# Kernel tuning notes

Hardware: AMD Instinct MI355X
Metric: run time of the kernel (lower is better)

## Reference

```python
import jax, jax.numpy as jnp
import numpy as np

B, TQ, TV, DQ, DV, UNITS = 4, 512, 1024, 256, 256, 64


def setup_inputs() -> dict:
    key = jax.random.key(0)
    k1, k2, k3, k4, k5 = jax.random.split(key, 5)
    return {
        "query": jax.random.normal(k1, (B, TQ, DQ), dtype=jnp.float32),
        "value": jax.random.normal(k2, (B, TV, DV), dtype=jnp.float32),
        "w1": jax.random.normal(k3, (DQ, UNITS), dtype=jnp.float32) / np.sqrt(DQ),
        "w2": jax.random.normal(k4, (DV, UNITS), dtype=jnp.float32) / np.sqrt(DV),
        "scale": jax.random.normal(k5, (UNITS,), dtype=jnp.float32),
    }


def reference(query, value, w1, w2, scale):
    # Dense projections (no bias)
    q = jnp.einsum('bqd,du->bqu', query, w1)   # [B,Tq,U]
    k = jnp.einsum('bvd,du->bvu', value, w2)   # [B,Tv,U]
    # Keras AdditiveAttention (use_scale=True):
    # scores[b,q,v] = sum_u scale[u] * tanh(q[b,q,u] + k[b,v,u])
    scores = jnp.einsum('bqvu,u->bqv',
                        jnp.tanh(q[:, :, None, :] + k[:, None, :, :]), scale)
    attn = jax.nn.softmax(scores, axis=-1)      # [B,Tq,Tv]
    context = jnp.einsum('bqv,bvd->bqd', attn, value)  # [B,Tq,Dv]
    return context, attn
```

## Files before the change

### kernel.cpp

```cpp
#include <hip/hip_runtime.h>
#include <math.h>

#define B 4
#define TQ 512
#define TV 1024
#define DQ 256
#define DV 256
#define UNITS 64
#define NQROW (B * TQ)
#define NKROW (B * TV)

#define CEXP  2.885390081777927f
#define LOG2E 1.4426950408889634f

__device__ __forceinline__ float fast_exp2(float x) {
#if __has_builtin(__builtin_amdgcn_exp2f)
    return __builtin_amdgcn_exp2f(x);
#else
    return __expf(0.6931471805599453f * x);
#endif
}

__device__ __forceinline__ float wave_sum(float v) {
    #pragma unroll
    for (int off = 32; off > 0; off >>= 1)
        v += __shfl_xor(v, off, 64);
    return v;
}

__device__ __forceinline__ unsigned short f2bf(float f) {
    unsigned int b = __float_as_uint(f);
    return (unsigned short)((b + 0x7fffu + ((b >> 16) & 1u)) >> 16);
}

#define RPB 8
__global__ __launch_bounds__(256) void proj_kernel(
        const float* __restrict__ query, const float* __restrict__ value,
        const float* __restrict__ w1, const float* __restrict__ w2,
        float* __restrict__ Eq, float* __restrict__ EkT,
        unsigned short* __restrict__ vbf) {
    __shared__ float rows[RPB][DQ];
    __shared__ float part[4][RPB][UNITS + 2];
    const int tid = threadIdx.x;
    const int u   = tid & 63;
    const int wid = tid >> 6;
    const int row0 = blockIdx.x * RPB;
    const bool isq = row0 < NQROW;
    const float* in = isq ? query + (size_t)row0 * DQ
                          : value + (size_t)(row0 - NQROW) * DQ;
    const float* w  = isq ? w1 : w2;

    {
        const float4* src = (const float4*)in;
        float4* dst = (float4*)&rows[0][0];
        dst[tid]       = src[tid];
        dst[tid + 256] = src[tid + 256];
    }
    __syncthreads();

    float a[RPB] = {};
    const int c0 = wid * 16;
    #pragma unroll 4
    for (int ci = 0; ci < 16; ++ci) {
        const int c = c0 + ci;
        const float w0v = w[(4 * c + 0) * UNITS + u];
        const float w1v = w[(4 * c + 1) * UNITS + u];
        const float w2v = w[(4 * c + 2) * UNITS + u];
        const float w3v = w[(4 * c + 3) * UNITS + u];
        #pragma unroll
        for (int r = 0; r < RPB; ++r) {
            const float4 t = *(const float4*)&rows[r][4 * c];
            a[r] = fmaf(t.x, w0v, a[r]);
            a[r] = fmaf(t.y, w1v, a[r]);
            a[r] = fmaf(t.z, w2v, a[r]);
            a[r] = fmaf(t.w, w3v, a[r]);
        }
    }
    #pragma unroll
    for (int r = 0; r < RPB; ++r)
        part[wid][r][u] = a[r];
    __syncthreads();

    if (isq) {
        #pragma unroll
        for (int h = 0; h < 2; ++h) {
            const int p = tid + h * 256;
            const int row = p >> 6, uu = p & 63;
            const float s = (part[0][row][uu] + part[1][row][uu]) +
                            (part[2][row][uu] + part[3][row][uu]);
            Eq[(size_t)(row0 + row) * UNITS + uu] = fast_exp2(CEXP * s);
        }
    } else {
        #pragma unroll
        for (int h = 0; h < 2; ++h) {
            const int p = tid + h * 256;
            const int uu = p >> 3, r = p & 7;
            const float s = (part[0][r][uu] + part[1][r][uu]) +
                            (part[2][r][uu] + part[3][r][uu]);
            EkT[(size_t)uu * NKROW + (row0 - NQROW) + r] = fast_exp2(CEXP * s);
        }
        const float* rf = &rows[0][0];
        const int base = tid * 8;
        uint4 pk;
        pk.x = (unsigned)f2bf(rf[base + 0]) | ((unsigned)f2bf(rf[base + 1]) << 16);
        pk.y = (unsigned)f2bf(rf[base + 2]) | ((unsigned)f2bf(rf[base + 3]) << 16);
        pk.z = (unsigned)f2bf(rf[base + 4]) | ((unsigned)f2bf(rf[base + 5]) << 16);
        pk.w = (unsigned)f2bf(rf[base + 6]) | ((unsigned)f2bf(rf[base + 7]) << 16);
        *(uint4*)(vbf + (size_t)(row0 - NQROW) * DV + base) = pk;
    }
}

#define QB 4
__global__ __launch_bounds__(512) void sc_kernel(
        const float* __restrict__ Eq,
        const float* __restrict__ EkT,
        const float* __restrict__ scale,
        const unsigned short* __restrict__ vbf,
        float* __restrict__ out_attn,
        float* __restrict__ out_ctx) {
    __shared__ float pool[QB * TV + 256 * QB * 4];
    __shared__ float q_lds[QB][UNITS];
    __shared__ float s_lds[UNITS];
    __shared__ float reds[QB][4];

    float* a_lds = pool;
    float4* scr  = (float4*)(pool + QB * TV);

    const int tid = threadIdx.x, lane = tid & 63, wid = tid >> 6;
    int bid = blockIdx.x;
    bid = (bid & 7) * ((NQROW / QB) >> 3) + (bid >> 3);
    const int b  = bid / (TQ / QB);
    const int q0 = (bid % (TQ / QB)) * QB;

    if (tid < QB * UNITS)
        q_lds[tid >> 6][tid & 63] =
            Eq[(size_t)(b * TQ + q0 + (tid >> 6)) * UNITS + (tid & 63)];
    else if (tid < QB * UNITS + UNITS)
        s_lds[tid - QB * UNITS] = scale[tid - QB * UNITS];
    __syncthreads();

    const int uh = tid >> 8;
    const int vt = tid & 255;
    const int ub = uh * 32;
    const float* ekc = EkT + (size_t)b * TV + 4 * vt + (size_t)ub * NKROW;
    float4 acc[QB];
    #pragma unroll
    for (int q = 0; q < QB; ++q) { acc[q].x = acc[q].y = acc[q].z = acc[q].w = 0.f; }

    #pragma unroll 2
    for (int u4 = 0; u4 < 8; ++u4) {
        const float4 ekA = *(const float4*)(ekc + (size_t)(4 * u4 + 0) * NKROW);
        const float4 ekB = *(const float4*)(ekc + (size_t)(4 * u4 + 1) * NKROW);
        const float4 ekC = *(const float4*)(ekc + (size_t)(4 * u4 + 2) * NKROW);
        const float4 ekD = *(const float4*)(ekc + (size_t)(4 * u4 + 3) * NKROW);
        const float4 s4 = *(const float4*)(s_lds + ub + 4 * u4);
        #pragma unroll
        for (int q = 0; q < QB; ++q) {
            const float4 eq = *(const float4*)(&q_lds[q][ub + 4 * u4]);
            #define EVAL(comp)                                                   \
            {                                                                    \
                float t0 = fmaf(eq.x, ekA.comp, 1.f);                            \
                float t1 = fmaf(eq.y, ekB.comp, 1.f);                            \
                float t2 = fmaf(eq.z, ekC.comp, 1.f);                            \
                float t3 = fmaf(eq.w, ekD.comp, 1.f);                            \
                float p01 = t0 * t1, p23 = t2 * t3;                              \
                float A  = fmaf(s4.y, t0, s4.x * t1);                            \
                float Bq = fmaf(s4.w, t2, s4.z * t3);                            \
                float num = fmaf(Bq, p01, A * p23);                              \
                float r = __builtin_amdgcn_rcpf(p01 * p23);                      \
                acc[q].comp = fmaf(num, r, acc[q].comp);                         \
            }
            EVAL(x) EVAL(y) EVAL(z) EVAL(w)
            #undef EVAL
        }
    }

    if (uh) {
        #pragma unroll
        for (int q = 0; q < QB; ++q)
            scr[vt * QB + q] = acc[q];
    }
    __syncthreads();

    float4 e[QB];
    if (!uh) {
        #pragma unroll
        for (int q = 0; q < QB; ++q) {
            const float4 t = scr[vt * QB + q];
            acc[q].x += t.x; acc[q].y += t.y; acc[q].z += t.z; acc[q].w += t.w;
            e[q].x = fast_exp2(-2.f * LOG2E * acc[q].x);
            e[q].y = fast_exp2(-2.f * LOG2E * acc[q].y);
            e[q].z = fast_exp2(-2.f * LOG2E * acc[q].z);
            e[q].w = fast_exp2(-2.f * LOG2E * acc[q].w);
            float s = wave_sum((e[q].x + e[q].y) + (e[q].z + e[q].w));
            if (lane == 0) reds[q][wid] = s;
        }
    }
    __syncthreads();
    if (!uh) {
        #pragma unroll
        for (int q = 0; q < QB; ++q) {
            const float ss = (reds[q][0] + reds[q][1]) + (reds[q][2] + reds[q][3]);
            const float inv = __builtin_amdgcn_rcpf(ss);
            float4 o;
            o.x = e[q].x * inv; o.y = e[q].y * inv;
            o.z = e[q].z * inv; o.w = e[q].w * inv;
            *(float4*)(a_lds + q * TV + 4 * vt) = o;
            *(float4*)(out_attn + (size_t)(b * TQ + q0 + q) * TV + 4 * vt) = o;
        }
    }
    __syncthreads();

    const int vq = tid >> 6;
    const int dp = tid & 63;
    const int d0 = dp * 4;
    const unsigned short* vb = vbf + ((size_t)b * TV + vq * 128) * DV + d0;
    float4 c[QB];
    #pragma unroll
    for (int q = 0; q < QB; ++q) { c[q].x = c[q].y = c[q].z = c[q].w = 0.f; }

    #pragma unroll 2
    for (int v4 = 0; v4 < 32; ++v4) {
        const int v = vq * 128 + v4 * 4;
        const float4 a0 = *(const float4*)(a_lds + 0 * TV + v);
        const float4 a1 = *(const float4*)(a_lds + 1 * TV + v);
        const float4 a2 = *(const float4*)(a_lds + 2 * TV + v);
        const float4 a3 = *(const float4*)(a_lds + 3 * TV + v);
        #define STEP(j, comp)                                                    \
        {                                                                        \
            const ushort4 wv = *(const ushort4*)(vb + (size_t)(v4 * 4 + j) * DV);\
            const float v0 = __uint_as_float((unsigned)wv.x << 16);              \
            const float v1 = __uint_as_float((unsigned)wv.y << 16);              \
            const float v2 = __uint_as_float((unsigned)wv.z << 16);              \
            const float v3 = __uint_as_float((unsigned)wv.w << 16);              \
            c[0].x = fmaf(a0.comp, v0, c[0].x); c[0].y = fmaf(a0.comp, v1, c[0].y); \
            c[0].z = fmaf(a0.comp, v2, c[0].z); c[0].w = fmaf(a0.comp, v3, c[0].w); \
            c[1].x = fmaf(a1.comp, v0, c[1].x); c[1].y = fmaf(a1.comp, v1, c[1].y); \
            c[1].z = fmaf(a1.comp, v2, c[1].z); c[1].w = fmaf(a1.comp, v3, c[1].w); \
            c[2].x = fmaf(a2.comp, v0, c[2].x); c[2].y = fmaf(a2.comp, v1, c[2].y); \
            c[2].z = fmaf(a2.comp, v2, c[2].z); c[2].w = fmaf(a2.comp, v3, c[2].w); \
            c[3].x = fmaf(a3.comp, v0, c[3].x); c[3].y = fmaf(a3.comp, v1, c[3].y); \
            c[3].z = fmaf(a3.comp, v2, c[3].z); c[3].w = fmaf(a3.comp, v3, c[3].w); \
        }
        STEP(0, x) STEP(1, y) STEP(2, z) STEP(3, w)
        #undef STEP
    }
    __syncthreads();

    if (vq != 0) {
        float* r = pool + (size_t)(vq - 1) * (QB * 64 * 4) + (0 * 64 + dp) * 4;
        #pragma unroll
        for (int q = 0; q < QB; ++q)
            *(float4*)(r + q * 64 * 4) = c[q];
    }
    __syncthreads();
    if (vq == 0) {
        #pragma unroll
        for (int g = 0; g < 7; ++g) {
            const float* r = pool + (size_t)g * (QB * 64 * 4) + dp * 4;
            #pragma unroll
            for (int q = 0; q < QB; ++q) {
                const float4 t = *(const float4*)(r + q * 64 * 4);
                c[q].x += t.x; c[q].y += t.y; c[q].z += t.z; c[q].w += t.w;
            }
        }
        #pragma unroll
        for (int q = 0; q < QB; ++q)
            *(float4*)(out_ctx + (size_t)(b * TQ + q0 + q) * DV + d0) = c[q];
    }
}

extern "C" void kernel_launch(void* const* d_in, const int* in_sizes, int n_in,
                              void* d_out, int out_size, void* d_ws, size_t ws_size,
                              hipStream_t stream) {
    const float* query = (const float*)d_in[0];
    const float* value = (const float*)d_in[1];
    const float* w1    = (const float*)d_in[2];
    const float* w2    = (const float*)d_in[3];
    const float* scale = (const float*)d_in[4];

    float* out      = (float*)d_out;
    float* out_ctx  = out;
    float* out_attn = out + (size_t)NQROW * DV;

    float* Eq  = (float*)d_ws;
    float* EkT = Eq + (size_t)NQROW * UNITS;
    unsigned short* vbf = (unsigned short*)(EkT + (size_t)UNITS * NKROW);

    proj_kernel<<<dim3((NQROW + NKROW) / RPB), 256, 0, stream>>>(
        query, value, w1, w2, Eq, EkT, vbf);
    sc_kernel<<<dim3(NQROW / QB), 512, 0, stream>>>(
        Eq, EkT, scale, vbf, out_attn, out_ctx);
}
```

Measured before the change: 43.46 us.

## Store exp(2k) in bf16 and split softmax epilogue across both thread halves

The projected key exponentials are now written as bf16 instead of fp32, which halves the bytes the score kernel reads from the EkT table. Each half of the block now finishes softmax for two of the four query rows, instead of one half sitting idle during the epilogue. The u-loop unroll goes from 2 to 4. The risk is lower precision in exp(2k) entering the tanh identity, which could hurt accuracy of the attention scores.

```diff
diff --git a/kernel.cpp b/kernel.cpp
--- a/kernel.cpp
+++ b/kernel.cpp
@@ -32,12 +32,15 @@
     unsigned int b = __float_as_uint(f);
     return (unsigned short)((b + 0x7fffu + ((b >> 16) & 1u)) >> 16);
 }
+__device__ __forceinline__ float bf2f(unsigned short u) {
+    return __uint_as_float((unsigned)u << 16);
+}
 
 #define RPB 8
 __global__ __launch_bounds__(256) void proj_kernel(
         const float* __restrict__ query, const float* __restrict__ value,
         const float* __restrict__ w1, const float* __restrict__ w2,
-        float* __restrict__ Eq, float* __restrict__ EkT,
+        float* __restrict__ Eq, unsigned short* __restrict__ ekbf,
         unsigned short* __restrict__ vbf) {
     __shared__ float rows[RPB][DQ];
     __shared__ float part[4][RPB][UNITS + 2];
@@ -97,7 +100,8 @@
             const int uu = p >> 3, r = p & 7;
             const float s = (part[0][r][uu] + part[1][r][uu]) +
                             (part[2][r][uu] + part[3][r][uu]);
-            EkT[(size_t)uu * NKROW + (row0 - NQROW) + r] = fast_exp2(CEXP * s);
+            ekbf[(size_t)uu * NKROW + (row0 - NQROW) + r] =
+                f2bf(fast_exp2(CEXP * s));
         }
         const float* rf = &rows[0][0];
         const int base = tid * 8;
@@ -113,7 +117,7 @@
 #define QB 4
 __global__ __launch_bounds__(512) void sc_kernel(
         const float* __restrict__ Eq,
-        const float* __restrict__ EkT,
+        const unsigned short* __restrict__ ekbf,
         const float* __restrict__ scale,
         const unsigned short* __restrict__ vbf,
         float* __restrict__ out_attn,
@@ -124,7 +128,8 @@
     __shared__ float reds[QB][4];
 
     float* a_lds = pool;
-    float4* scr  = (float4*)(pool + QB * TV);
+    float4* scr0 = (float4*)(pool + QB * TV);
+    float4* scr1 = (float4*)(pool + QB * TV + 256 * 8);
 
     const int tid = threadIdx.x, lane = tid & 63, wid = tid >> 6;
     int bid = blockIdx.x;
@@ -142,17 +147,22 @@
     const int uh = tid >> 8;
     const int vt = tid & 255;
     const int ub = uh * 32;
-    const float* ekc = EkT + (size_t)b * TV + 4 * vt + (size_t)ub * NKROW;
+    const unsigned short* ekc = ekbf + (size_t)b * TV + 4 * vt + (size_t)ub * NKROW;
     float4 acc[QB];
     #pragma unroll
     for (int q = 0; q < QB; ++q) { acc[q].x = acc[q].y = acc[q].z = acc[q].w = 0.f; }
 
-    #pragma unroll 2
+    #pragma unroll 4
     for (int u4 = 0; u4 < 8; ++u4) {
-        const float4 ekA = *(const float4*)(ekc + (size_t)(4 * u4 + 0) * NKROW);
-        const float4 ekB = *(const float4*)(ekc + (size_t)(4 * u4 + 1) * NKROW);
-        const float4 ekC = *(const float4*)(ekc + (size_t)(4 * u4 + 2) * NKROW);
-        const float4 ekD = *(const float4*)(ekc + (size_t)(4 * u4 + 3) * NKROW);
+        const ushort4 wA = *(const ushort4*)(ekc + (size_t)(4 * u4 + 0) * NKROW);
+        const ushort4 wB = *(const ushort4*)(ekc + (size_t)(4 * u4 + 1) * NKROW);
+        const ushort4 wC = *(const ushort4*)(ekc + (size_t)(4 * u4 + 2) * NKROW);
+        const ushort4 wD = *(const ushort4*)(ekc + (size_t)(4 * u4 + 3) * NKROW);
+        float4 ekA, ekB, ekC, ekD;
+        ekA.x = bf2f(wA.x); ekA.y = bf2f(wA.y); ekA.z = bf2f(wA.z); ekA.w = bf2f(wA.w);
+        ekB.x = bf2f(wB.x); ekB.y = bf2f(wB.y); ekB.z = bf2f(wB.z); ekB.w = bf2f(wB.w);
+        ekC.x = bf2f(wC.x); ekC.y = bf2f(wC.y); ekC.z = bf2f(wC.z); ekC.w = bf2f(wC.w);
+        ekD.x = bf2f(wD.x); ekD.y = bf2f(wD.y); ekD.z = bf2f(wD.z); ekD.w = bf2f(wD.w);
         const float4 s4 = *(const float4*)(s_lds + ub + 4 * u4);
         #pragma unroll
         for (int q = 0; q < QB; ++q) {
@@ -176,38 +186,41 @@
     }
 
     if (uh) {
-        #pragma unroll
-        for (int q = 0; q < QB; ++q)
-            scr[vt * QB + q] = acc[q];
-    }
-    __syncthreads();
-
-    float4 e[QB];
-    if (!uh) {
-        #pragma unroll
-        for (int q = 0; q < QB; ++q) {
-            const float4 t = scr[vt * QB + q];
-            acc[q].x += t.x; acc[q].y += t.y; acc[q].z += t.z; acc[q].w += t.w;
-            e[q].x = fast_exp2(-2.f * LOG2E * acc[q].x);
-            e[q].y = fast_exp2(-2.f * LOG2E * acc[q].y);
-            e[q].z = fast_exp2(-2.f * LOG2E * acc[q].z);
-            e[q].w = fast_exp2(-2.f * LOG2E * acc[q].w);
-            float s = wave_sum((e[q].x + e[q].y) + (e[q].z + e[q].w));
-            if (lane == 0) reds[q][wid] = s;
-        }
-    }
-    __syncthreads();
-    if (!uh) {
-        #pragma unroll
-        for (int q = 0; q < QB; ++q) {
-            const float ss = (reds[q][0] + reds[q][1]) + (reds[q][2] + reds[q][3]);
-            const float inv = __builtin_amdgcn_rcpf(ss);
-            float4 o;
-            o.x = e[q].x * inv; o.y = e[q].y * inv;
-            o.z = e[q].z * inv; o.w = e[q].w * inv;
-            *(float4*)(a_lds + q * TV + 4 * vt) = o;
-            *(float4*)(out_attn + (size_t)(b * TQ + q0 + q) * TV + 4 * vt) = o;
-        }
+        scr1[vt * 2 + 0] = acc[0];
+        scr1[vt * 2 + 1] = acc[1];
+    } else {
+        scr0[vt * 2 + 0] = acc[2];
+        scr0[vt * 2 + 1] = acc[3];
+    }
+    __syncthreads();
+
+    const int qa = uh * 2;
+    float4 e[2];
+    #pragma unroll
+    for (int j = 0; j < 2; ++j) {
+        const int q = qa + j;
+        const float4 t = uh ? scr0[vt * 2 + j] : scr1[vt * 2 + j];
+        float4 s;
+        s.x = acc[q].x + t.x; s.y = acc[q].y + t.y;
+        s.z = acc[q].z + t.z; s.w = acc[q].w + t.w;
+        e[j].x = fast_exp2(-2.f * LOG2E * s.x);
+        e[j].y = fast_exp2(-2.f * LOG2E * s.y);
+        e[j].z = fast_exp2(-2.f * LOG2E * s.z);
+        e[j].w = fast_exp2(-2.f * LOG2E * s.w);
+        float sm = wave_sum((e[j].x + e[j].y) + (e[j].z + e[j].w));
+        if (lane == 0) reds[q][wid & 3] = sm;
+    }
+    __syncthreads();
+    #pragma unroll
+    for (int j = 0; j < 2; ++j) {
+        const int q = qa + j;
+        const float ss = (reds[q][0] + reds[q][1]) + (reds[q][2] + reds[q][3]);
+        const float inv = __builtin_amdgcn_rcpf(ss);
+        float4 o;
+        o.x = e[j].x * inv; o.y = e[j].y * inv;
+        o.z = e[j].z * inv; o.w = e[j].w * inv;
+        *(float4*)(a_lds + q * TV + 4 * vt) = o;
+        *(float4*)(out_attn + (size_t)(b * TQ + q0 + q) * TV + 4 * vt) = o;
     }
     __syncthreads();
 
@@ -229,10 +242,10 @@
         #define STEP(j, comp)                                                    \
         {                                                                        \
             const ushort4 wv = *(const ushort4*)(vb + (size_t)(v4 * 4 + j) * DV);\
-            const float v0 = __uint_as_float((unsigned)wv.x << 16);              \
-            const float v1 = __uint_as_float((unsigned)wv.y << 16);              \
-            const float v2 = __uint_as_float((unsigned)wv.z << 16);              \
-            const float v3 = __uint_as_float((unsigned)wv.w << 16);              \
+            const float v0 = bf2f(wv.x);                                         \
+            const float v1 = bf2f(wv.y);                                         \
+            const float v2 = bf2f(wv.z);                                         \
+            const float v3 = bf2f(wv.w);                                         \
             c[0].x = fmaf(a0.comp, v0, c[0].x); c[0].y = fmaf(a0.comp, v1, c[0].y); \
             c[0].z = fmaf(a0.comp, v2, c[0].z); c[0].w = fmaf(a0.comp, v3, c[0].w); \
             c[1].x = fmaf(a1.comp, v0, c[1].x); c[1].y = fmaf(a1.comp, v1, c[1].y); \
@@ -248,7 +261,7 @@
     __syncthreads();
 
     if (vq != 0) {
-        float* r = pool + (size_t)(vq - 1) * (QB * 64 * 4) + (0 * 64 + dp) * 4;
+        float* r = pool + (size_t)(vq - 1) * (QB * 64 * 4) + dp * 4;
         #pragma unroll
         for (int q = 0; q < QB; ++q)
             *(float4*)(r + q * 64 * 4) = c[q];
@@ -284,11 +297,11 @@
     float* out_attn = out + (size_t)NQROW * DV;
 
     float* Eq  = (float*)d_ws;
-    float* EkT = Eq + (size_t)NQROW * UNITS;
-    unsigned short* vbf = (unsigned short*)(EkT + (size_t)UNITS * NKROW);
+    unsigned short* ekbf = (unsigned short*)(Eq + (size_t)NQROW * UNITS);
+    unsigned short* vbf  = ekbf + (size_t)UNITS * NKROW;
 
     proj_kernel<<<dim3((NQROW + NKROW) / RPB), 256, 0, stream>>>(
-        query, value, w1, w2, Eq, EkT, vbf);
+        query, value, w1, w2, Eq, ekbf, vbf);
     sc_kernel<<<dim3(NQROW / QB), 512, 0, stream>>>(
-        Eq, EkT, scale, vbf, out_attn, out_ctx);
-}
+        Eq, ekbf, scale, vbf, out_attn, out_ctx);
+}
```

New measurement: 47.19 us. 8.6% more time.
